# Optimization experiments

Measured on AMD Instinct MI355X. Metric: run time of the kernel, lower is better.

## Reference

```python
import jax, jax.numpy as jnp
import numpy as np

BAG, SEQ, D = 8, 512, 768      # docs per bag, seq len, bert hidden (d_model)
NB = 4                          # bridge spans kept per doc (subsampling cap regime)
NPD = 2 + NB                    # nodes per doc: h, t, bridges
N = BAG * NPD                   # total entity nodes in the bag graph (48)
T = N * N                       # matrix cells fed to MatTransformer (2304)
H = 8
DK = D // H                     # head dim 96
DFF, L = 1024, 4                # MatTransformer ffn width / num_layers
NREL = 97                       # num_relations (DocRED)
EPS = 1e-5


def _ln(x, g, b):
    m = jnp.mean(x, axis=-1, keepdims=True)
    v = jnp.var(x, axis=-1, keepdims=True)
    return (x - m) * jax.lax.rsqrt(v + EPS) * g + b


def setup_inputs() -> dict:
    key = jax.random.key(0)
    ks = jax.random.split(key, 16)
    s = 0.02
    p = {}
    # stand-in for BERT last hidden states
    p['embedding'] = jax.random.normal(ks[0], (BAG, SEQ, D), jnp.float32)
    # entity spans per doc: [h, t, b1..bNB] x (start, end) inclusive, from get_htb markers
    starts = jax.random.randint(ks[1], (BAG, NPD), 0, SEQ - 9)
    lens = jax.random.randint(ks[2], (BAG, NPD), 1, 9)
    p['spans'] = jnp.stack([starts, starts + lens - 1], axis=-1).astype(jnp.int32)
    # pairwise relation encoders wu / wv / ln1
    p['Wu'] = jax.random.normal(ks[3], (D, D)) * s; p['bu'] = jnp.zeros((D,))
    p['Wv'] = jax.random.normal(ks[4], (D, D)) * s; p['bv'] = jnp.zeros((D,))
    p['Wl'] = jax.random.normal(ks[5], (D, D)) * s; p['bl'] = jnp.zeros((D,))
    # MatTransformer: L layers of MHA + FFN, params stacked over layers
    p['Wq'] = jax.random.normal(ks[6], (L, D, D)) * s;  p['bq'] = jnp.zeros((L, D))
    p['Wk'] = jax.random.normal(ks[7], (L, D, D)) * s;  p['bk'] = jnp.zeros((L, D))
    p['Wvm'] = jax.random.normal(ks[8], (L, D, D)) * s; p['bvm'] = jnp.zeros((L, D))
    p['Wo'] = jax.random.normal(ks[9], (L, D, D)) * s;  p['bo'] = jnp.zeros((L, D))
    p['F1'] = jax.random.normal(ks[10], (L, D, DFF)) * s; p['f1'] = jnp.zeros((L, DFF))
    p['F2'] = jax.random.normal(ks[11], (L, DFF, D)) * s; p['f2'] = jnp.zeros((L, D))
    p['g1'] = jnp.ones((L, D)); p['be1'] = jnp.zeros((L, D))
    p['g2'] = jnp.ones((L, D)); p['be2'] = jnp.zeros((L, D))
    # final norm + predictor
    p['ng'] = jnp.ones((D,)); p['nb'] = jnp.zeros((D,))
    p['Wp'] = jax.random.normal(ks[12], (D, NREL)) * s; p['bp'] = jnp.zeros((NREL,))
    return p


def _forward(embedding, spans, Wu, bu, Wv, bv, Wl, bl, Wq, bq, Wk, bk, Wvm, bvm,
             Wo, bo, F1, f1, F2, f2, g1, be1, g2, be2, ng, nb, Wp, bp):
    # --- ragged span gather + max pooling (masked max, vectorized) ---
    pos = jnp.arange(SEQ)
    m = (pos >= spans[..., :1]) & (pos <= spans[..., 1:])          # [BAG, NPD, SEQ]
    neg = jnp.finfo(embedding.dtype).min
    pooled = jnp.max(jnp.where(m[..., None], embedding[:, None, :, :], neg), axis=2)  # [BAG, NPD, D]
    htb = pooled.reshape(N, D)                                      # h/t/bridge node embs
    # --- pairwise outer-sum relation encoding: relu(ln1(relu(u_i + v_j))) ---
    u = htb @ Wu + bu
    v = htb @ Wv + bv
    rel = jax.nn.relu(jax.nn.relu(u[:, None, :] + v[None, :, :]) @ Wl + bl)  # [N, N, D]
    # --- MatTransformer: multi-head self-attention over the N*N matrix cells ---
    x = rel.reshape(T, D)
    scale = 1.0 / np.sqrt(DK).astype(np.float32)
    for l in range(L):
        q = (x @ Wq[l] + bq[l]).reshape(T, H, DK)
        k = (x @ Wk[l] + bk[l]).reshape(T, H, DK)
        vv = (x @ Wvm[l] + bvm[l]).reshape(T, H, DK)
        att = jax.nn.softmax(jnp.einsum('qhd,khd->hqk', q, k) * scale, axis=-1)
        o = jnp.einsum('hqk,khd->qhd', att, vv).reshape(T, D) @ Wo[l] + bo[l]
        x = _ln(x + o, g1[l], be1[l])
        f = jax.nn.relu(x @ F1[l] + f1[l]) @ F2[l] + f2[l]
        x = _ln(x + f, g2[l], be2[l])
    rel_m = x.reshape(N, N, D)
    # --- gather (h_pos, t_pos) cells: h at i*NPD, t at i*NPD+1 ---
    hp = jnp.arange(BAG) * NPD
    t_feature = rel_m[hp, hp + 1]                                   # [BAG, D]
    ht_logits = _ln(t_feature, ng, nb) @ Wp + bp                    # [BAG, NREL]
    bag_logit = jnp.max(ht_logits, axis=0, keepdims=True)           # [1, NREL]
    return bag_logit, ht_logits


def reference(embedding, spans, Wu, bu, Wv, bv, Wl, bl, Wq, bq, Wk, bk, Wvm, bvm,
              Wo, bo, F1, f1, F2, f2, g1, be1, g2, be2, ng, nb, Wp, bp):
    return _forward(embedding, spans, Wu, bu, Wv, bv, Wl, bl, Wq, bq, Wk, bk,
                    Wvm, bvm, Wo, bo, F1, f1, F2, f2, g1, be1, g2, be2, ng, nb, Wp, bp)
```

## Files before the change

kernel.cpp:

```cpp
#include <hip/hip_runtime.h>
#include <hip/hip_bf16.h>

typedef __hip_bfloat16 bf16;
typedef __bf16 bf16x8 __attribute__((ext_vector_type(8)));
typedef float f32x4 __attribute__((ext_vector_type(4)));

#define BAG 8
#define SEQ 512
#define DM 768
#define NPD 6
#define NNODE 48
#define TT 2304
#define NH 8
#define DKH 96
#define DFF 1024
#define NLAYER 4
#define NREL 97
#define SP 6
#define KSPAN (TT / SP)
#define LN_EPS 1e-5f

__device__ __forceinline__ float b2f(const bf16 x) { return __bfloat162float(x); }
__device__ __forceinline__ bf16 f2b(float f) { return __float2bfloat16(f); }
__device__ __forceinline__ unsigned short f2bu(float f) {
    bf16 h = __float2bfloat16(f);
    return *reinterpret_cast<unsigned short*>(&h);
}

__global__ __launch_bounds__(256) void span_pool(const float* __restrict__ emb,
                                                 const int* __restrict__ spans,
                                                 bf16* __restrict__ htb) {
    const int n = blockIdx.x;
    const int b = n / NPD;
    int s0 = spans[n * 2 + 0];
    int s1 = spans[n * 2 + 1];
    s0 = min(max(s0, 0), SEQ - 1);
    s1 = min(max(s1, s0), SEQ - 1);
    const float* base = emb + (size_t)b * SEQ * DM;
    for (int d = threadIdx.x; d < DM; d += 256) {
        float m = -3.0e38f;
        for (int s = s0; s <= s1; ++s) m = fmaxf(m, base[(size_t)s * DM + d]);
        htb[(size_t)n * DM + d] = f2b(m);
    }
}

__global__ __launch_bounds__(256) void prep_wt3(const float* __restrict__ W0,
                                                const float* __restrict__ W1,
                                                const float* __restrict__ W2,
                                                bf16* __restrict__ Wt) {
    __shared__ __align__(16) __bf16 tile[64][72];
    const int z = blockIdx.z;
    const float* W = (z == 0) ? W0 : (z == 1) ? W1 : W2;
    bf16* out = Wt + (size_t)z * DM * DM;
    const int t = threadIdx.x;
    const int k0 = blockIdx.x * 64, n0 = blockIdx.y * 64;
    const int r = t >> 2, cg = (t & 3) * 16;
#pragma unroll
    for (int i = 0; i < 4; ++i) {
        const float4 v = *(const float4*)&W[(size_t)(k0 + r) * DM + n0 + cg + 4 * i];
        tile[r][cg + 4 * i + 0] = (__bf16)v.x;
        tile[r][cg + 4 * i + 1] = (__bf16)v.y;
        tile[r][cg + 4 * i + 2] = (__bf16)v.z;
        tile[r][cg + 4 * i + 3] = (__bf16)v.w;
    }
    __syncthreads();
#pragma unroll
    for (int i = 0; i < 2; ++i) {
        bf16x8 o;
#pragma unroll
        for (int j = 0; j < 8; ++j) o[j] = tile[cg + 8 * i + j][r];
        *(bf16x8*)&out[(size_t)(n0 + r) * DM + k0 + cg + 8 * i] = o;
    }
}

__global__ __launch_bounds__(256) void prep6(const float* __restrict__ Wq,
                                             const float* __restrict__ Wk,
                                             const float* __restrict__ Wv,
                                             const float* __restrict__ Wo,
                                             const float* __restrict__ F1,
                                             const float* __restrict__ F2,
                                             bf16* __restrict__ slab) {
    __shared__ __align__(16) __bf16 tile[64][72];
    const int z = blockIdx.z;
    int K = DM, N = DM;
    const float* W;
    size_t off;
    switch (z) {
        case 0: W = Wq; off = 0;       break;
        case 1: W = Wk; off = 589824;  break;
        case 2: W = Wv; off = 1179648; break;
        case 3: W = Wo; off = 1769472; break;
        case 4: W = F1; off = 2359296; N = DFF; break;
        default: W = F2; off = 3145728; K = DFF; break;
    }
    const int k0 = blockIdx.x * 64, n0 = blockIdx.y * 64;
    if (k0 >= K || n0 >= N) return;
    bf16* out = slab + off;
    const int t = threadIdx.x;
    const int r = t >> 2, cg = (t & 3) * 16;
#pragma unroll
    for (int i = 0; i < 4; ++i) {
        const float4 v = *(const float4*)&W[(size_t)(k0 + r) * N + n0 + cg + 4 * i];
        tile[r][cg + 4 * i + 0] = (__bf16)v.x;
        tile[r][cg + 4 * i + 1] = (__bf16)v.y;
        tile[r][cg + 4 * i + 2] = (__bf16)v.z;
        tile[r][cg + 4 * i + 3] = (__bf16)v.w;
    }
    __syncthreads();
#pragma unroll
    for (int i = 0; i < 2; ++i) {
        bf16x8 o;
#pragma unroll
        for (int j = 0; j < 8; ++j) o[j] = tile[cg + 8 * i + j][r];
        *(bf16x8*)&out[(size_t)(n0 + r) * K + k0 + cg + 8 * i] = o;
    }
}

template <int RELU>
__global__ __launch_bounds__(128) void gemm_bt(const bf16* __restrict__ A,
                                               const bf16* __restrict__ Bt,
                                               const float* __restrict__ bias,
                                               bf16* __restrict__ C,
                                               int M, int N, int K) {
    __shared__ __align__(16) __bf16 As[2][32][72];
    __shared__ __align__(16) __bf16 Bs[2][64][72];
    const int t = threadIdx.x;
    const int w = t >> 6, lane = t & 63;
    const int quad = lane >> 4, l15 = lane & 15;
    const int row0 = blockIdx.y * 32, col0 = blockIdx.x * 64;
    const int a_row = t >> 2, a_oct = (t & 3) * 8;
    const int b_row = t >> 1, b_base = (t & 1) * 8;
    const bool a_ok = (row0 + a_row) < M;

    const f32x4 fz = {0.f, 0.f, 0.f, 0.f};
    f32x4 acc[4];
#pragma unroll
    for (int i = 0; i < 4; ++i) acc[i] = fz;

    bf16x8 av0, av1, bv[4];
    if (a_ok) {
        av0 = *(const bf16x8*)&A[(size_t)(row0 + a_row) * K + a_oct];
        av1 = *(const bf16x8*)&A[(size_t)(row0 + a_row) * K + 32 + a_oct];
    } else {
        for (int j = 0; j < 8; ++j) { av0[j] = (__bf16)0.0f; av1[j] = (__bf16)0.0f; }
    }
#pragma unroll
    for (int j = 0; j < 4; ++j)
        bv[j] = *(const bf16x8*)&Bt[(size_t)(col0 + b_row) * K + b_base + 16 * j];

    int cur = 0;
    for (int k0 = 0; k0 < K; k0 += 64) {
        *(bf16x8*)&As[cur][a_row][a_oct] = av0;
        *(bf16x8*)&As[cur][a_row][32 + a_oct] = av1;
#pragma unroll
        for (int j = 0; j < 4; ++j) *(bf16x8*)&Bs[cur][b_row][b_base + 16 * j] = bv[j];
        __syncthreads();

        if (k0 + 64 < K) {
            if (a_ok) {
                av0 = *(const bf16x8*)&A[(size_t)(row0 + a_row) * K + k0 + 64 + a_oct];
                av1 = *(const bf16x8*)&A[(size_t)(row0 + a_row) * K + k0 + 96 + a_oct];
            }
#pragma unroll
            for (int j = 0; j < 4; ++j)
                bv[j] = *(const bf16x8*)&Bt[(size_t)(col0 + b_row) * K + k0 + 64 + b_base + 16 * j];
        }

#pragma unroll
        for (int kk = 0; kk < 2; ++kk) {
            const bf16x8 af = *(const bf16x8*)&As[cur][16 * w + l15][quad * 8 + 32 * kk];
#pragma unroll
            for (int nt = 0; nt < 4; ++nt) {
                const bf16x8 bfv = *(const bf16x8*)&Bs[cur][16 * nt + l15][quad * 8 + 32 * kk];
                acc[nt] = __builtin_amdgcn_mfma_f32_16x16x32_bf16(af, bfv, acc[nt], 0, 0, 0);
            }
        }
        cur ^= 1;
    }

#pragma unroll
    for (int nt = 0; nt < 4; ++nt) {
        const int col = col0 + 16 * nt + l15;
        const float bvl = bias[col];
#pragma unroll
        for (int r = 0; r < 4; ++r) {
            const int row = row0 + 16 * w + quad * 4 + r;
            if (row < M) {
                float v = acc[nt][r] + bvl;
                if (RELU) v = fmaxf(v, 0.f);
                C[(size_t)row * N + col] = f2b(v);
            }
        }
    }
}

__global__ __launch_bounds__(128) void gemm_qkv(const bf16* __restrict__ A,
                                                const bf16* __restrict__ Bt,
                                                const float* __restrict__ b0,
                                                const float* __restrict__ b1,
                                                const float* __restrict__ b2,
                                                bf16* __restrict__ C0,
                                                bf16* __restrict__ C1,
                                                bf16* __restrict__ Vt) {
    __shared__ __align__(16) __bf16 As[32][72];
    __shared__ __align__(16) __bf16 Bs[64][72];
    const int t = threadIdx.x;
    const int w = t >> 6, lane = t & 63;
    const int quad = lane >> 4, l15 = lane & 15;
    const int row0 = blockIdx.y * 32, col0 = blockIdx.x * 64;
    const int a_row = t >> 2, a_oct = (t & 3) * 8;
    const int b_row = t >> 1, b_base = (t & 1) * 8;

    const f32x4 fz = {0.f, 0.f, 0.f, 0.f};
    f32x4 acc[4];
#pragma unroll
    for (int i = 0; i < 4; ++i) acc[i] = fz;

    bf16x8 av0, av1, bv[4];
    av0 = *(const bf16x8*)&A[(size_t)(row0 + a_row) * DM + a_oct];
    av1 = *(const bf16x8*)&A[(size_t)(row0 + a_row) * DM + 32 + a_oct];
#pragma unroll
    for (int j = 0; j < 4; ++j)
        bv[j] = *(const bf16x8*)&Bt[(size_t)(col0 + b_row) * DM + b_base + 16 * j];

    for (int k0 = 0; k0 < DM; k0 += 64) {
        *(bf16x8*)&As[a_row][a_oct] = av0;
        *(bf16x8*)&As[a_row][32 + a_oct] = av1;
#pragma unroll
        for (int j = 0; j < 4; ++j) *(bf16x8*)&Bs[b_row][b_base + 16 * j] = bv[j];
        __syncthreads();

        if (k0 + 64 < DM) {
            av0 = *(const bf16x8*)&A[(size_t)(row0 + a_row) * DM + k0 + 64 + a_oct];
            av1 = *(const bf16x8*)&A[(size_t)(row0 + a_row) * DM + k0 + 96 + a_oct];
#pragma unroll
            for (int j = 0; j < 4; ++j)
                bv[j] = *(const bf16x8*)&Bt[(size_t)(col0 + b_row) * DM + k0 + 64 + b_base + 16 * j];
        }

#pragma unroll
        for (int kk = 0; kk < 2; ++kk) {
            const bf16x8 af = *(const bf16x8*)&As[16 * w + l15][quad * 8 + 32 * kk];
#pragma unroll
            for (int nt = 0; nt < 4; ++nt) {
                const bf16x8 bfv = *(const bf16x8*)&Bs[16 * nt + l15][quad * 8 + 32 * kk];
                acc[nt] = __builtin_amdgcn_mfma_f32_16x16x32_bf16(af, bfv, acc[nt], 0, 0, 0);
            }
        }
        __syncthreads();
    }

    const int buf = col0 / DM;
    const int lc0 = col0 - buf * DM;
    if (buf < 2) {
        bf16* Cb = (buf == 0) ? C0 : C1;
        const float* bb = (buf == 0) ? b0 : b1;
#pragma unroll
        for (int nt = 0; nt < 4; ++nt) {
            const int col = lc0 + 16 * nt + l15;
            const float bvl = bb[col];
#pragma unroll
            for (int r = 0; r < 4; ++r) {
                const int row = row0 + 16 * w + quad * 4 + r;
                Cb[(size_t)row * DM + col] = f2b(acc[nt][r] + bvl);
            }
        }
    } else {
#pragma unroll
        for (int nt = 0; nt < 4; ++nt) {
            const float bvl = b2[lc0 + 16 * nt + l15];
#pragma unroll
            for (int r = 0; r < 4; ++r)
                Bs[16 * nt + l15][16 * w + quad * 4 + r] = (__bf16)(acc[nt][r] + bvl);
        }
        __syncthreads();
        const int c = t >> 1, half = (t & 1) * 16;
        const bf16x8 o0 = *(const bf16x8*)&Bs[c][half];
        const bf16x8 o1 = *(const bf16x8*)&Bs[c][half + 8];
        *(bf16x8*)&Vt[(size_t)(lc0 + c) * TT + row0 + half] = o0;
        *(bf16x8*)&Vt[(size_t)(lc0 + c) * TT + row0 + half + 8] = o1;
    }
}

template <int RELU>
__global__ __launch_bounds__(128) void gemm_mfma(const bf16* __restrict__ A,
                                                 const float* __restrict__ W,
                                                 const float* __restrict__ bias,
                                                 bf16* __restrict__ C,
                                                 int M, int N, int K) {
    __shared__ __align__(16) __bf16 As[32][40];
    __shared__ __align__(16) __bf16 Bs[64][40];
    const int t = threadIdx.x;
    const int w = t >> 6, lane = t & 63;
    const int quad = lane >> 4, l15 = lane & 15;
    const int row0 = blockIdx.y * 32, col0 = blockIdx.x * 64;
    const int s_row = t >> 2, s_kg = (t & 3) * 8;
    const int s_colg = (t & 15) * 4, s_kp = t >> 4;
    const bool a_ok = (row0 + s_row) < M;
    const f32x4 fz = {0.f, 0.f, 0.f, 0.f};
    f32x4 acc[4];
#pragma unroll
    for (int i = 0; i < 4; ++i) acc[i] = fz;

    for (int k0 = 0; k0 < K; k0 += 32) {
        bf16x8 av;
        for (int j = 0; j < 8; ++j) av[j] = (__bf16)0.0f;
        if (a_ok) av = *(const bf16x8*)&A[(size_t)(row0 + s_row) * K + k0 + s_kg];
        *(bf16x8*)&As[s_row][s_kg] = av;
#pragma unroll
        for (int rep = 0; rep < 2; ++rep) {
            const int kp = s_kp + 8 * rep;
            const size_t gb = (size_t)(k0 + 2 * kp) * N + col0 + s_colg;
            const float4 w0 = *(const float4*)&W[gb];
            const float4 w1 = *(const float4*)&W[gb + N];
#pragma unroll
            for (int i = 0; i < 4; ++i) {
                ushort2 pk;
                pk.x = f2bu((&w0.x)[i]);
                pk.y = f2bu((&w1.x)[i]);
                *(ushort2*)&Bs[s_colg + i][2 * kp] = pk;
            }
        }
        __syncthreads();
        const bf16x8 af = *(const bf16x8*)&As[16 * w + l15][quad * 8];
#pragma unroll
        for (int nt = 0; nt < 4; ++nt) {
            const bf16x8 bfv = *(const bf16x8*)&Bs[16 * nt + l15][quad * 8];
            acc[nt] = __builtin_amdgcn_mfma_f32_16x16x32_bf16(af, bfv, acc[nt], 0, 0, 0);
        }
        __syncthreads();
    }
#pragma unroll
    for (int nt = 0; nt < 4; ++nt) {
        const int col = col0 + 16 * nt + l15;
        const float bvl = bias[col];
#pragma unroll
        for (int r = 0; r < 4; ++r) {
            const int row = row0 + 16 * w + quad * 4 + r;
            if (row < M) {
                float v = acc[nt][r] + bvl;
                if (RELU) v = fmaxf(v, 0.f);
                C[(size_t)row * N + col] = f2b(v);
            }
        }
    }
}

__global__ __launch_bounds__(256) void build_relA(const bf16* __restrict__ u,
                                                  const bf16* __restrict__ v,
                                                  bf16* __restrict__ A) {
    const int cell = blockIdx.x;
    const int i = cell / NNODE, j = cell % NNODE;
    for (int k = threadIdx.x; k < DM; k += 256) {
        A[(size_t)cell * DM + k] = f2b(fmaxf(b2f(u[i * DM + k]) + b2f(v[j * DM + k]), 0.f));
    }
}

__global__ __launch_bounds__(256) void transpose_v(const bf16* __restrict__ v,
                                                   bf16* __restrict__ vt) {
    __shared__ __align__(16) __bf16 tile[64][72];
    const int t = threadIdx.x;
    const int bx = blockIdx.x, by = blockIdx.y;
    const int r = t >> 2, cg = (t & 3) * 16;
#pragma unroll
    for (int i = 0; i < 2; ++i)
        *(bf16x8*)&tile[r][cg + 8 * i] =
            *(const bf16x8*)&v[(size_t)(by * 64 + r) * DM + bx * 64 + cg + 8 * i];
    __syncthreads();
#pragma unroll
    for (int i = 0; i < 2; ++i) {
        bf16x8 o;
#pragma unroll
        for (int j = 0; j < 8; ++j) o[j] = tile[cg + 8 * i + j][r];
        *(bf16x8*)&vt[(size_t)(bx * 64 + r) * TT + by * 64 + cg + 8 * i] = o;
    }
}

template <int MODE>
__global__ __launch_bounds__(256) void attn_mfma(const bf16* __restrict__ qb,
                                                 const bf16* __restrict__ kb,
                                                 const bf16* __restrict__ vtb,
                                                 bf16* __restrict__ ob,
                                                 bf16* __restrict__ Opb,
                                                 float* __restrict__ Lp,
                                                 int kspan) {
    __shared__ __align__(16) __bf16 Ks[64][104];
    __shared__ __align__(16) __bf16 Vts[96][72];
    __shared__ __align__(16) __bf16 Ps[4][16][72];

    const int t = threadIdx.x;
    const int w = t >> 6, lane = t & 63;
    const int quad = lane >> 4, l15 = lane & 15;
    const int h = blockIdx.y;
    const int q0 = blockIdx.x * 64;
    const int p = blockIdx.z;
    const int kstart = p * kspan;
    const float scale = 0.10206207261596575f;

    bf16x8 qf[3];
#pragma unroll
    for (int ks = 0; ks < 3; ++ks) {
        qf[ks] = *(const bf16x8*)&qb[(size_t)(q0 + 16 * w + l15) * DM + h * DKH + quad * 8 + 32 * ks];
#pragma unroll
        for (int j = 0; j < 8; ++j) qf[ks][j] = (__bf16)((float)qf[ks][j] * scale);
    }

    const f32x4 fz = {0.f, 0.f, 0.f, 0.f};
    f32x4 Oa[6];
#pragma unroll
    for (int i = 0; i < 6; ++i) Oa[i] = fz;
    float lrow[4] = {0.f, 0.f, 0.f, 0.f};

    bf16x8 kreg[3], vreg[3];
#pragma unroll
    for (int i = 0; i < 3; ++i) {
        const int idx = t + 256 * i;
        const int r = idx / 12, c = idx % 12;
        kreg[i] = *(const bf16x8*)&kb[(size_t)(kstart + r) * DM + h * DKH + c * 8];
        const int d = idx >> 3, ck = idx & 7;
        vreg[i] = *(const bf16x8*)&vtb[(size_t)(h * DKH + d) * TT + kstart + ck * 8];
    }

    for (int kc = kstart; kc < kstart + kspan; kc += 64) {
        __syncthreads();
#pragma unroll
        for (int i = 0; i < 3; ++i) {
            const int idx = t + 256 * i;
            const int r = idx / 12, c = idx % 12;
            *(bf16x8*)&Ks[r][c * 8] = kreg[i];
            const int d = idx >> 3, ck = idx & 7;
            *(bf16x8*)&Vts[d][ck * 8] = vreg[i];
        }
        __syncthreads();

        if (kc + 64 < kstart + kspan) {
#pragma unroll
            for (int i = 0; i < 3; ++i) {
                const int idx = t + 256 * i;
                const int r = idx / 12, c = idx % 12;
                kreg[i] = *(const bf16x8*)&kb[(size_t)(kc + 64 + r) * DM + h * DKH + c * 8];
                const int d = idx >> 3, ck = idx & 7;
                vreg[i] = *(const bf16x8*)&vtb[(size_t)(h * DKH + d) * TT + kc + 64 + ck * 8];
            }
        }

        f32x4 Sa[4] = {fz, fz, fz, fz};
#pragma unroll
        for (int nt = 0; nt < 4; ++nt)
#pragma unroll
            for (int ks = 0; ks < 3; ++ks) {
                const bf16x8 kf = *(const bf16x8*)&Ks[l15 + 16 * nt][quad * 8 + 32 * ks];
                Sa[nt] = __builtin_amdgcn_mfma_f32_16x16x32_bf16(qf[ks], kf, Sa[nt], 0, 0, 0);
            }

#pragma unroll
        for (int r = 0; r < 4; ++r) {
            const float p0 = __expf(Sa[0][r]), p1 = __expf(Sa[1][r]);
            const float p2 = __expf(Sa[2][r]), p3 = __expf(Sa[3][r]);
            Ps[w][quad * 4 + r][l15]      = (__bf16)p0;
            Ps[w][quad * 4 + r][l15 + 16] = (__bf16)p1;
            Ps[w][quad * 4 + r][l15 + 32] = (__bf16)p2;
            Ps[w][quad * 4 + r][l15 + 48] = (__bf16)p3;
            float ps = p0 + p1 + p2 + p3;
            ps += __shfl_xor(ps, 1);
            ps += __shfl_xor(ps, 2);
            ps += __shfl_xor(ps, 4);
            ps += __shfl_xor(ps, 8);
            lrow[r] += ps;
        }

        const bf16x8 pa0 = *(const bf16x8*)&Ps[w][l15][quad * 8];
        const bf16x8 pa1 = *(const bf16x8*)&Ps[w][l15][32 + quad * 8];

#pragma unroll
        for (int nt = 0; nt < 6; ++nt) {
            const bf16x8 vf0 = *(const bf16x8*)&Vts[l15 + 16 * nt][quad * 8];
            const bf16x8 vf1 = *(const bf16x8*)&Vts[l15 + 16 * nt][32 + quad * 8];
            Oa[nt] = __builtin_amdgcn_mfma_f32_16x16x32_bf16(pa0, vf0, Oa[nt], 0, 0, 0);
            Oa[nt] = __builtin_amdgcn_mfma_f32_16x16x32_bf16(pa1, vf1, Oa[nt], 0, 0, 0);
        }
    }

    if (MODE == 0) {
#pragma unroll
        for (int nt = 0; nt < 6; ++nt)
#pragma unroll
            for (int r = 0; r < 4; ++r) {
                const int row = q0 + 16 * w + quad * 4 + r;
                ob[(size_t)row * DM + h * DKH + 16 * nt + l15] = f2b(Oa[nt][r] / lrow[r]);
            }
    } else {
#pragma unroll
        for (int nt = 0; nt < 6; ++nt)
#pragma unroll
            for (int r = 0; r < 4; ++r) {
                const int row = q0 + 16 * w + quad * 4 + r;
                Opb[((size_t)p * TT + row) * DM + h * DKH + 16 * nt + l15] = f2b(Oa[nt][r]);
            }
        if (l15 == 0) {
#pragma unroll
            for (int r = 0; r < 4; ++r) {
                const int row = q0 + 16 * w + quad * 4 + r;
                Lp[((size_t)p * NH + h) * TT + row] = lrow[r];
            }
        }
    }
}

__global__ __launch_bounds__(256) void attn_merge(const bf16* __restrict__ Opb,
                                                  const float* __restrict__ Lp,
                                                  bf16* __restrict__ ob) {
    __shared__ float Ls[NH];
    const int row = blockIdx.x, t = threadIdx.x;
    if (t < NH) {
        float L = 0.f;
#pragma unroll
        for (int p = 0; p < SP; ++p) L += Lp[((size_t)p * NH + t) * TT + row];
        Ls[t] = 1.0f / L;
    }
    __syncthreads();
#pragma unroll
    for (int i = 0; i < 3; ++i) {
        const int d = t + 256 * i;
        const int h = d / DKH;
        float o = 0.f;
#pragma unroll
        for (int p = 0; p < SP; ++p)
            o += b2f(Opb[((size_t)p * TT + row) * DM + d]);
        ob[(size_t)row * DM + d] = f2b(o * Ls[h]);
    }
}

__global__ __launch_bounds__(256) void add_ln(bf16* __restrict__ x,
                                              const bf16* __restrict__ r,
                                              const float* __restrict__ g,
                                              const float* __restrict__ be) {
    __shared__ float red[4];
    const int row = blockIdx.x;
    bf16* xr = x + (size_t)row * DM;
    const bf16* rr = r + (size_t)row * DM;
    const int t = threadIdx.x;

    float v0 = b2f(xr[t]) + b2f(rr[t]);
    float v1 = b2f(xr[t + 256]) + b2f(rr[t + 256]);
    float v2 = b2f(xr[t + 512]) + b2f(rr[t + 512]);
    float s = v0 + v1 + v2;
#pragma unroll
    for (int off = 32; off >= 1; off >>= 1) s += __shfl_xor(s, off);
    if ((t & 63) == 0) red[t >> 6] = s;
    __syncthreads();
    s = red[0] + red[1] + red[2] + red[3];
    const float mean = s * (1.f / 768.f);
    __syncthreads();

    const float d0 = v0 - mean, d1 = v1 - mean, d2 = v2 - mean;
    float ss = d0 * d0 + d1 * d1 + d2 * d2;
#pragma unroll
    for (int off = 32; off >= 1; off >>= 1) ss += __shfl_xor(ss, off);
    if ((t & 63) == 0) red[t >> 6] = ss;
    __syncthreads();
    ss = red[0] + red[1] + red[2] + red[3];
    const float inv = rsqrtf(ss * (1.f / 768.f) + LN_EPS);

    xr[t]       = f2b(d0 * inv * g[t]       + be[t]);
    xr[t + 256] = f2b(d1 * inv * g[t + 256] + be[t + 256]);
    xr[t + 512] = f2b(d2 * inv * g[t + 512] + be[t + 512]);
}

__global__ __launch_bounds__(256) void predict(const bf16* __restrict__ x,
                                               const float* __restrict__ ng,
                                               const float* __restrict__ nb,
                                               const float* __restrict__ Wp,
                                               const float* __restrict__ bp,
                                               float* __restrict__ out) {
    __shared__ float xs[BAG][DM];
    __shared__ float red[4][BAG];
    const int t = threadIdx.x;
    const int rel = blockIdx.x;
    const int wid = t >> 6, lane = t & 63;

    for (int rep = 0; rep < 2; ++rep) {
        const int b = wid + rep * 4;
        const bf16* row = x + (size_t)(294 * b + 1) * DM;
        float vals[12];
        float s = 0.f;
#pragma unroll
        for (int i = 0; i < 12; ++i) { vals[i] = b2f(row[lane + i * 64]); s += vals[i]; }
#pragma unroll
        for (int off = 32; off >= 1; off >>= 1) s += __shfl_xor(s, off);
        const float mean = s * (1.f / 768.f);
        float ss = 0.f;
#pragma unroll
        for (int i = 0; i < 12; ++i) { const float d = vals[i] - mean; ss += d * d; }
#pragma unroll
        for (int off = 32; off >= 1; off >>= 1) ss += __shfl_xor(ss, off);
        const float inv = rsqrtf(ss * (1.f / 768.f) + LN_EPS);
#pragma unroll
        for (int i = 0; i < 12; ++i) {
            const int d = lane + i * 64;
            xs[b][d] = (vals[i] - mean) * inv * ng[d] + nb[d];
        }
    }
    __syncthreads();

    float pb[BAG];
#pragma unroll
    for (int b = 0; b < BAG; ++b) pb[b] = 0.f;
    for (int k = t; k < DM; k += 256) {
        const float wv = Wp[(size_t)k * NREL + rel];
#pragma unroll
        for (int b = 0; b < BAG; ++b) pb[b] += xs[b][k] * wv;
    }
#pragma unroll
    for (int b = 0; b < BAG; ++b)
#pragma unroll
        for (int off = 32; off >= 1; off >>= 1) pb[b] += __shfl_xor(pb[b], off);
    if (lane == 0)
#pragma unroll
        for (int b = 0; b < BAG; ++b) red[wid][b] = pb[b];
    __syncthreads();
    if (t == 0) {
        float mx = -3.0e38f;
        for (int b = 0; b < BAG; ++b) {
            const float v = red[0][b] + red[1][b] + red[2][b] + red[3][b] + bp[rel];
            out[NREL + b * NREL + rel] = v;
            mx = fmaxf(mx, v);
        }
        out[rel] = mx;
    }
}

extern "C" void kernel_launch(void* const* d_in, const int* in_sizes, int n_in,
                              void* d_out, int out_size, void* d_ws, size_t ws_size,
                              hipStream_t stream) {
    const float* emb  = (const float*)d_in[0];
    const int* spans  = (const int*)d_in[1];
    const float* Wu = (const float*)d_in[2];  const float* bu = (const float*)d_in[3];
    const float* Wv = (const float*)d_in[4];  const float* bv = (const float*)d_in[5];
    const float* Wl = (const float*)d_in[6];  const float* bl = (const float*)d_in[7];
    const float* Wq = (const float*)d_in[8];  const float* bq = (const float*)d_in[9];
    const float* Wk = (const float*)d_in[10]; const float* bk = (const float*)d_in[11];
    const float* Wvm = (const float*)d_in[12]; const float* bvm = (const float*)d_in[13];
    const float* Wo = (const float*)d_in[14]; const float* bo = (const float*)d_in[15];
    const float* F1 = (const float*)d_in[16]; const float* f1 = (const float*)d_in[17];
    const float* F2 = (const float*)d_in[18]; const float* f2 = (const float*)d_in[19];
    const float* g1 = (const float*)d_in[20]; const float* be1 = (const float*)d_in[21];
    const float* g2 = (const float*)d_in[22]; const float* be2 = (const float*)d_in[23];
    const float* ng = (const float*)d_in[24]; const float* nb = (const float*)d_in[25];
    const float* Wp = (const float*)d_in[26]; const float* bp = (const float*)d_in[27];

    char* wsb = (char*)d_ws;
    bf16* htb = (bf16*)(wsb + 0);
    bf16* ub  = (bf16*)(wsb + 73728);
    bf16* vbn = (bf16*)(wsb + 147456);
    bf16* x   = (bf16*)(wsb + 221184);
    bf16* Bq  = (bf16*)(wsb + 3760128);
    bf16* Bk  = (bf16*)(wsb + 7299072);
    bf16* Bv  = (bf16*)(wsb + 10838016);
    bf16* Vt  = (bf16*)(wsb + 15556608);
    bf16* slab = (bf16*)(wsb + 19095552);
    bf16* Opb = (bf16*)(wsb + 26959872);
    float* Lp = (float*)(wsb + 48193536);

    const size_t FULL_END = 48635904;
    const bool use_full = ws_size >= FULL_END;

    span_pool<<<NNODE, 256, 0, stream>>>(emb, spans, htb);

    if (use_full) {
        prep_wt3<<<dim3(12, 12, 3), 256, 0, stream>>>(Wu, Wv, Wl, slab);
        gemm_bt<0><<<dim3(12, 2), 128, 0, stream>>>(htb, slab, bu, ub, NNODE, DM, DM);
        gemm_bt<0><<<dim3(12, 2), 128, 0, stream>>>(htb, slab + 589824, bv, vbn, NNODE, DM, DM);
        build_relA<<<TT, 256, 0, stream>>>(ub, vbn, Bq);
        gemm_bt<1><<<dim3(12, TT / 32), 128, 0, stream>>>(Bq, slab + 1179648, bl, x, TT, DM, DM);

        for (int l = 0; l < NLAYER; ++l) {
            const size_t wo = (size_t)l * DM * DM;
            const size_t f1o = (size_t)l * DM * DFF;
            prep6<<<dim3(16, 16, 6), 256, 0, stream>>>(Wq + wo, Wk + wo, Wvm + wo,
                                                       Wo + wo, F1 + f1o, F2 + f1o, slab);
            gemm_qkv<<<dim3(36, TT / 32), 128, 0, stream>>>(x, slab, bq + l * DM, bk + l * DM,
                                                            bvm + l * DM, Bq, Bk, Vt);
            attn_mfma<1><<<dim3(TT / 64, NH, SP), 256, 0, stream>>>(Bq, Bk, Vt, Bq, Opb, Lp, KSPAN);
            attn_merge<<<TT, 256, 0, stream>>>(Opb, Lp, Bq);
            gemm_bt<0><<<dim3(12, TT / 32), 128, 0, stream>>>(Bq, slab + 1769472, bo + l * DM, Bk, TT, DM, DM);
            add_ln<<<TT, 256, 0, stream>>>(x, Bk, g1 + l * DM, be1 + l * DM);
            gemm_bt<1><<<dim3(16, TT / 32), 128, 0, stream>>>(x, slab + 2359296, f1 + l * DFF, Bv, TT, DFF, DM);
            gemm_bt<0><<<dim3(12, TT / 32), 128, 0, stream>>>(Bv, slab + 3145728, f2 + l * DM, Bk, TT, DM, DFF);
            add_ln<<<TT, 256, 0, stream>>>(x, Bk, g2 + l * DM, be2 + l * DM);
        }
    } else {
        gemm_mfma<0><<<dim3(12, 2), 128, 0, stream>>>(htb, Wu, bu, ub, NNODE, DM, DM);
        gemm_mfma<0><<<dim3(12, 2), 128, 0, stream>>>(htb, Wv, bv, vbn, NNODE, DM, DM);
        build_relA<<<TT, 256, 0, stream>>>(ub, vbn, Bq);
        gemm_mfma<1><<<dim3(12, TT / 32), 128, 0, stream>>>(Bq, Wl, bl, x, TT, DM, DM);

        for (int l = 0; l < NLAYER; ++l) {
            const size_t wo = (size_t)l * DM * DM;
            const size_t f1o = (size_t)l * DM * DFF;
            gemm_mfma<0><<<dim3(12, TT / 32), 128, 0, stream>>>(x, Wq + wo, bq + l * DM, Bq, TT, DM, DM);
            gemm_mfma<0><<<dim3(12, TT / 32), 128, 0, stream>>>(x, Wk + wo, bk + l * DM, Bk, TT, DM, DM);
            gemm_mfma<0><<<dim3(12, TT / 32), 128, 0, stream>>>(x, Wvm + wo, bvm + l * DM, Bv, TT, DM, DM);
            transpose_v<<<dim3(DM / 64, TT / 64), 256, 0, stream>>>(Bv, Vt);
            attn_mfma<0><<<dim3(TT / 64, NH, 1), 256, 0, stream>>>(Bq, Bk, Vt, Bq, Opb, Lp, TT);
            gemm_mfma<0><<<dim3(12, TT / 32), 128, 0, stream>>>(Bq, Wo + wo, bo + l * DM, Bk, TT, DM, DM);
            add_ln<<<TT, 256, 0, stream>>>(x, Bk, g1 + l * DM, be1 + l * DM);
            gemm_mfma<1><<<dim3(16, TT / 32), 128, 0, stream>>>(x, F1 + f1o, f1 + l * DFF, Bv, TT, DFF, DM);
            gemm_mfma<0><<<dim3(12, TT / 32), 128, 0, stream>>>(Bv, F2 + f1o, f2 + l * DM, Bk, TT, DM, DFF);
            add_ln<<<TT, 256, 0, stream>>>(x, Bk, g2 + l * DM, be2 + l * DM);
        }
    }

    predict<<<NREL, 256, 0, stream>>>(x, ng, nb, Wp, bp, (float*)d_out);
}
```

Measured before the change: 713.3 us.

## Double-buffer K tile, load V fragments directly from global, vectorize attention merge

The attention kernel now double-buffers the K tile in shared memory, which removes one of the two barriers per key chunk. It also drops the V shared-memory tile: each lane loads its V^T fragments straight from global memory into registers. The merge kernel now handles 8 rows per block with 8-wide bf16 vector loads and stores instead of scalar accesses. The intent is to cut barrier and LDS traffic and to improve memory efficiency, at the cost of more per-lane global loads and higher register pressure (launch bounds set to 4 waves per SIMD).

```diff
diff --git a/kernel.cpp b/kernel.cpp
--- a/kernel.cpp
+++ b/kernel.cpp
@@ -377,15 +377,14 @@
 }
 
 template <int MODE>
-__global__ __launch_bounds__(256) void attn_mfma(const bf16* __restrict__ qb,
-                                                 const bf16* __restrict__ kb,
-                                                 const bf16* __restrict__ vtb,
-                                                 bf16* __restrict__ ob,
-                                                 bf16* __restrict__ Opb,
-                                                 float* __restrict__ Lp,
-                                                 int kspan) {
-    __shared__ __align__(16) __bf16 Ks[64][104];
-    __shared__ __align__(16) __bf16 Vts[96][72];
+__global__ __launch_bounds__(256, 4) void attn_mfma(const bf16* __restrict__ qb,
+                                                    const bf16* __restrict__ kb,
+                                                    const bf16* __restrict__ vtb,
+                                                    bf16* __restrict__ ob,
+                                                    bf16* __restrict__ Opb,
+                                                    float* __restrict__ Lp,
+                                                    int kspan) {
+    __shared__ __align__(16) __bf16 Ks[2][64][104];
     __shared__ __align__(16) __bf16 Ps[4][16][72];
 
     const int t = threadIdx.x;
@@ -395,6 +394,7 @@
     const int q0 = blockIdx.x * 64;
     const int p = blockIdx.z;
     const int kstart = p * kspan;
+    const int kend = kstart + kspan;
     const float scale = 0.10206207261596575f;
 
     bf16x8 qf[3];
@@ -411,47 +411,66 @@
     for (int i = 0; i < 6; ++i) Oa[i] = fz;
     float lrow[4] = {0.f, 0.f, 0.f, 0.f};
 
-    bf16x8 kreg[3], vreg[3];
+    const bf16* vrow = vtb + (size_t)(h * DKH + l15) * TT + quad * 8;
+
+    const int kr = (t * 3) / 12, kc0 = (t * 3) % 12;
+
+    bf16x8 kreg[3];
 #pragma unroll
     for (int i = 0; i < 3; ++i) {
         const int idx = t + 256 * i;
         const int r = idx / 12, c = idx % 12;
         kreg[i] = *(const bf16x8*)&kb[(size_t)(kstart + r) * DM + h * DKH + c * 8];
-        const int d = idx >> 3, ck = idx & 7;
-        vreg[i] = *(const bf16x8*)&vtb[(size_t)(h * DKH + d) * TT + kstart + ck * 8];
-    }
-
-    for (int kc = kstart; kc < kstart + kspan; kc += 64) {
-        __syncthreads();
-#pragma unroll
-        for (int i = 0; i < 3; ++i) {
-            const int idx = t + 256 * i;
-            const int r = idx / 12, c = idx % 12;
-            *(bf16x8*)&Ks[r][c * 8] = kreg[i];
-            const int d = idx >> 3, ck = idx & 7;
-            *(bf16x8*)&Vts[d][ck * 8] = vreg[i];
-        }
-        __syncthreads();
-
-        if (kc + 64 < kstart + kspan) {
+    }
+#pragma unroll
+    for (int i = 0; i < 3; ++i) {
+        const int idx = t + 256 * i;
+        const int r = idx / 12, c = idx % 12;
+        *(bf16x8*)&Ks[0][r][c * 8] = kreg[i];
+    }
+
+    int cur = 0;
+    for (int kc = kstart; kc < kend; kc += 64) {
+        const bool hasnext = (kc + 64) < kend;
+
+        bf16x8 vf0[6];
+#pragma unroll
+        for (int nt = 0; nt < 6; ++nt)
+            vf0[nt] = *(const bf16x8*)&vrow[(size_t)(16 * nt) * TT + kc];
+
+        if (hasnext) {
 #pragma unroll
             for (int i = 0; i < 3; ++i) {
                 const int idx = t + 256 * i;
                 const int r = idx / 12, c = idx % 12;
                 kreg[i] = *(const bf16x8*)&kb[(size_t)(kc + 64 + r) * DM + h * DKH + c * 8];
-                const int d = idx >> 3, ck = idx & 7;
-                vreg[i] = *(const bf16x8*)&vtb[(size_t)(h * DKH + d) * TT + kc + 64 + ck * 8];
-            }
-        }
+            }
+        }
+
+        __syncthreads();
 
         f32x4 Sa[4] = {fz, fz, fz, fz};
 #pragma unroll
         for (int nt = 0; nt < 4; ++nt)
 #pragma unroll
             for (int ks = 0; ks < 3; ++ks) {
-                const bf16x8 kf = *(const bf16x8*)&Ks[l15 + 16 * nt][quad * 8 + 32 * ks];
+                const bf16x8 kf = *(const bf16x8*)&Ks[cur][l15 + 16 * nt][quad * 8 + 32 * ks];
                 Sa[nt] = __builtin_amdgcn_mfma_f32_16x16x32_bf16(qf[ks], kf, Sa[nt], 0, 0, 0);
             }
+
+        if (hasnext) {
+#pragma unroll
+            for (int i = 0; i < 3; ++i) {
+                const int idx = t + 256 * i;
+                const int r = idx / 12, c = idx % 12;
+                *(bf16x8*)&Ks[cur ^ 1][r][c * 8] = kreg[i];
+            }
+        }
+
+        bf16x8 vf1[6];
+#pragma unroll
+        for (int nt = 0; nt < 6; ++nt)
+            vf1[nt] = *(const bf16x8*)&vrow[(size_t)(16 * nt) * TT + kc + 32];
 
 #pragma unroll
         for (int r = 0; r < 4; ++r) {
@@ -473,12 +492,13 @@
         const bf16x8 pa1 = *(const bf16x8*)&Ps[w][l15][32 + quad * 8];
 
 #pragma unroll
-        for (int nt = 0; nt < 6; ++nt) {
-            const bf16x8 vf0 = *(const bf16x8*)&Vts[l15 + 16 * nt][quad * 8];
-            const bf16x8 vf1 = *(const bf16x8*)&Vts[l15 + 16 * nt][32 + quad * 8];
-            Oa[nt] = __builtin_amdgcn_mfma_f32_16x16x32_bf16(pa0, vf0, Oa[nt], 0, 0, 0);
-            Oa[nt] = __builtin_amdgcn_mfma_f32_16x16x32_bf16(pa1, vf1, Oa[nt], 0, 0, 0);
-        }
+        for (int nt = 0; nt < 6; ++nt)
+            Oa[nt] = __builtin_amdgcn_mfma_f32_16x16x32_bf16(pa0, vf0[nt], Oa[nt], 0, 0, 0);
+#pragma unroll
+        for (int nt = 0; nt < 6; ++nt)
+            Oa[nt] = __builtin_amdgcn_mfma_f32_16x16x32_bf16(pa1, vf1[nt], Oa[nt], 0, 0, 0);
+
+        cur ^= 1;
     }
 
     if (MODE == 0) {
@@ -510,24 +530,36 @@
 __global__ __launch_bounds__(256) void attn_merge(const bf16* __restrict__ Opb,
                                                   const float* __restrict__ Lp,
                                                   bf16* __restrict__ ob) {
-    __shared__ float Ls[NH];
-    const int row = blockIdx.x, t = threadIdx.x;
-    if (t < NH) {
+    __shared__ float Ls[8][NH];
+    const int r0 = blockIdx.x * 8;
+    const int t = threadIdx.x;
+    if (t < 8 * NH) {
+        const int rl = t >> 3, hh = t & 7;
         float L = 0.f;
 #pragma unroll
-        for (int p = 0; p < SP; ++p) L += Lp[((size_t)p * NH + t) * TT + row];
-        Ls[t] = 1.0f / L;
-    }
-    __syncthreads();
-#pragma unroll
-    for (int i = 0; i < 3; ++i) {
-        const int d = t + 256 * i;
-        const int h = d / DKH;
-        float o = 0.f;
-#pragma unroll
-        for (int p = 0; p < SP; ++p)
-            o += b2f(Opb[((size_t)p * TT + row) * DM + d]);
-        ob[(size_t)row * DM + d] = f2b(o * Ls[h]);
+        for (int p = 0; p < SP; ++p) L += Lp[((size_t)p * NH + hh) * TT + r0 + rl];
+        Ls[rl][hh] = 1.0f / L;
+    }
+    __syncthreads();
+    const int rl = t >> 5, lane = t & 31;
+    const int row = r0 + rl;
+#pragma unroll
+    for (int j = 0; j < 3; ++j) {
+        const int d0 = lane * 8 + j * 256;
+        float acc[8];
+#pragma unroll
+        for (int e = 0; e < 8; ++e) acc[e] = 0.f;
+#pragma unroll
+        for (int p = 0; p < SP; ++p) {
+            const bf16x8 vv = *(const bf16x8*)&Opb[((size_t)p * TT + row) * DM + d0];
+#pragma unroll
+            for (int e = 0; e < 8; ++e) acc[e] += (float)vv[e];
+        }
+        const float s = Ls[rl][d0 / DKH];
+        bf16x8 o;
+#pragma unroll
+        for (int e = 0; e < 8; ++e) o[e] = (__bf16)(acc[e] * s);
+        *(bf16x8*)&ob[(size_t)row * DM + d0] = o;
     }
 }
 
@@ -682,7 +714,7 @@
             gemm_qkv<<<dim3(36, TT / 32), 128, 0, stream>>>(x, slab, bq + l * DM, bk + l * DM,
                                                             bvm + l * DM, Bq, Bk, Vt);
             attn_mfma<1><<<dim3(TT / 64, NH, SP), 256, 0, stream>>>(Bq, Bk, Vt, Bq, Opb, Lp, KSPAN);
-            attn_merge<<<TT, 256, 0, stream>>>(Opb, Lp, Bq);
+            attn_merge<<<TT / 8, 256, 0, stream>>>(Opb, Lp, Bq);
             gemm_bt<0><<<dim3(12, TT / 32), 128, 0, stream>>>(Bq, slab + 1769472, bo + l * DM, Bk, TT, DM, DM);
             add_ln<<<TT, 256, 0, stream>>>(x, Bk, g1 + l * DM, be1 + l * DM);
             gemm_bt<1><<<dim3(16, TT / 32), 128, 0, stream>>>(x, slab + 2359296, f1 + l * DFF, Bv, TT, DFF, DM);
```

Measured after the change: 907.7 us. 27.3% more time.
